# Kernel optimization log

Measured on AMD Instinct MI355X. Metric: run time of the kernel, lower is better.

The kernel has to match this reference:

```python
import jax, jax.numpy as jnp
import numpy as np
from jax import lax

# quantization bit widths (config)
IB, WB, RB, AB = 8, 4, 4, 8


def quantize(x, bw):
    """Signed fixed-point quantization to bw bits in [-1, 1) with STE."""
    scale = 2.0 ** (bw - 1)
    q = jnp.clip(jnp.round(x * scale), -scale, scale - 1) / scale
    return x + lax.stop_gradient(q - x)


def setup_inputs() -> dict:
    key = jax.random.key(0)
    k1, k2, k3, k4, k5 = jax.random.split(key, 5)
    B, T, I, H, O = 256, 1024, 64, 256, 16
    inputs = jax.random.normal(k1, (B, T, I), dtype=jnp.float32)
    # input kernel init: uniform(-1, 1)
    Wi = jax.random.uniform(k2, (H, I), dtype=jnp.float32, minval=-1.0, maxval=1.0)
    # recurrent kernel: orthogonal (geotorch parametrization); materialize via QR
    A = jax.random.normal(k3, (H, H), dtype=jnp.float32)
    Wr, _ = jnp.linalg.qr(A)
    Wr = Wr.astype(jnp.float32)
    Wo = jax.random.normal(k4, (O, H), dtype=jnp.float32) * 0.1
    b = jax.random.normal(k5, (H,), dtype=jnp.float32) * 0.01
    return {"inputs": inputs, "Wi": Wi, "Wr": Wr, "Wo": Wo, "b": b}


def reference(inputs, Wi, Wr, Wo, b):
    # quantize inputs (ib bits)
    x = quantize(inputs, IB)
    # quantized input projection, precomputed for all timesteps: [B,T,H]
    u = jnp.einsum("bti,hi->bth", x, quantize(Wi, WB))
    Wrq = quantize(Wr, RB)  # quantized orthogonal recurrent weight [H,H]
    B = inputs.shape[0]
    H = Wr.shape[0]
    h0 = jnp.zeros((B, H), dtype=inputs.dtype)

    def step(h, u_t):
        z = u_t + h @ Wrq.T                      # [B,H]
        m = jax.nn.relu(jnp.abs(z) + b)          # modrelu magnitude
        h_new = quantize(jnp.sign(z) * m, AB)    # quantized activation
        return h_new, None

    u_t = jnp.swapaxes(u, 0, 1)  # [T,B,H]
    h_last, _ = lax.scan(step, h0, u_t)
    # output head on last hidden state
    out = h_last @ quantize(Wo, WB).T  # [B,O]
    return out
```

## Files before the change

### kernel.cpp

```cpp
#include <hip/hip_runtime.h>


#define TSEQ 1024
#define IDIM 64
#define HDIM 256
#define ODIM 16

using i32x4 = __attribute__((ext_vector_type(4))) int;

__device__ __forceinline__ int sdot4i8(int a, int b, int c) {
#if __has_builtin(__builtin_amdgcn_sdot4)
    return __builtin_amdgcn_sdot4(a, b, c, false);
#else
    int r = c;
    r += ((a << 24) >> 24) * ((b << 24) >> 24);
    r += ((a << 16) >> 24) * ((b << 16) >> 24);
    r += ((a << 8)  >> 24) * ((b << 8)  >> 24);
    r += (a >> 24) * (b >> 24);
    return r;
#endif
}

__device__ __forceinline__ int qpack4(float4 f, float s, float lo, float hi) {
    int a = (int)fminf(fmaxf(rintf(f.x * s), lo), hi);
    int b = (int)fminf(fmaxf(rintf(f.y * s), lo), hi);
    int c = (int)fminf(fmaxf(rintf(f.z * s), lo), hi);
    int d = (int)fminf(fmaxf(rintf(f.w * s), lo), hi);
    return (a & 255) | ((b & 255) << 8) | ((c & 255) << 16) | ((d & 255) << 24);
}

__global__ __launch_bounds__(256, 1)
void qornn_kernel(const float* __restrict__ x, const float* __restrict__ Wi,
                  const float* __restrict__ Wr, const float* __restrict__ Wo,
                  const float* __restrict__ bias, float* __restrict__ out) {
    __shared__ alignas(16) int xlds[TSEQ * 16 + 16];
    __shared__ alignas(16) int wstage[8192];
    __shared__ alignas(16) int hbuf[2][64];

    const int tid = threadIdx.x;
    const int brow = blockIdx.x;
    const int w   = tid >> 6;
    const int l   = tid & 63;
    const int lm  = l & 15;
    const int lg  = l >> 4;
    const int olocal = ((l & 15) >> 2) * 16 + lg * 4 + (l & 3);
    const int oglob  = w * 64 + olocal;

    {
        const float4* wi4 = (const float4*)Wi;
        #pragma unroll
        for (int it = 0; it < 16; ++it) {
            int flat = it * 256 + tid;
            wstage[flat] = qpack4(wi4[flat], 8.0f, -8.0f, 7.0f);
        }
    }
    __syncthreads();
    int4 wi[4];
    {
        const int4* p = (const int4*)wstage;
        #pragma unroll
        for (int i = 0; i < 4; ++i) wi[i] = p[oglob * 4 + i];
    }
    __syncthreads();

    i32x4 wrA[4][4];
    {
        const float4* wr4 = (const float4*)Wr;
        #pragma unroll
        for (int it = 0; it < 32; ++it) {
            int flat = it * 256 + tid;
            wstage[flat] = qpack4(wr4[flat], 8.0f, -8.0f, 7.0f);
        }
        __syncthreads();
        if (w < 2) {
            const i32x4* p = (const i32x4*)wstage;
            #pragma unroll
            for (int tt = 0; tt < 4; ++tt)
                #pragma unroll
                for (int s = 0; s < 4; ++s)
                    wrA[tt][s] = p[(w * 64 + tt * 16 + lm) * 16 + s * 4 + lg];
        }
        __syncthreads();
        #pragma unroll
        for (int it = 0; it < 32; ++it) {
            int flat = it * 256 + tid;
            wstage[flat] = qpack4(wr4[8192 + flat], 8.0f, -8.0f, 7.0f);
        }
        __syncthreads();
        if (w >= 2) {
            const i32x4* p = (const i32x4*)wstage;
            #pragma unroll
            for (int tt = 0; tt < 4; ++tt)
                #pragma unroll
                for (int s = 0; s < 4; ++s)
                    wrA[tt][s] = p[((w - 2) * 64 + tt * 16 + lm) * 16 + s * 4 + lg];
        }
        __syncthreads();
    }

    {
        const float4* wo4 = (const float4*)Wo;
        #pragma unroll
        for (int it = 0; it < 4; ++it) {
            int flat = it * 256 + tid;
            wstage[flat] = qpack4(wo4[flat], 8.0f, -8.0f, 7.0f);
        }
    }

    {
        const float4* rowf4 = (const float4*)(x + (size_t)brow * (TSEQ * IDIM));
        #pragma unroll 8
        for (int it = 0; it < 64; ++it) {
            int flat = it * 256 + tid;
            xlds[flat] = qpack4(rowf4[flat], 128.0f, -128.0f, 127.0f);
        }
    }
    if (tid < 64) hbuf[0][tid] = 0;
    __syncthreads();

    const float bv = bias[oglob];
    const bool tb1 = (l & 8) != 0;
    const bool tb0 = (l & 4) != 0;
    const bool rb1 = (l & 2) != 0;
    const bool rb0 = (l & 1) != 0;

    int u = 0;
    #pragma unroll
    for (int s = 0; s < 4; ++s) {
        const int4 xx = ((const int4*)xlds)[s];
        u = sdot4i8(xx.x, wi[s].x, u);
        u = sdot4i8(xx.y, wi[s].y, u);
        u = sdot4i8(xx.z, wi[s].z, u);
        u = sdot4i8(xx.w, wi[s].w, u);
    }

    const i32x4 zero4 = {0, 0, 0, 0};

    #pragma unroll 2
    for (int t = 0; t < TSEQ; ++t) {
        i32x4 hB[4];
        {
            const i32x4* hP = (const i32x4*)hbuf[t & 1];
            #pragma unroll
            for (int s = 0; s < 4; ++s) hB[s] = hP[s * 4 + lg];
        }
        int4 xn[4];
        #pragma unroll
        for (int s = 0; s < 4; ++s) xn[s] = ((const int4*)xlds)[(t + 1) * 4 + s];

        i32x4 c0 = zero4, c1 = zero4, c2 = zero4, c3 = zero4;
        #pragma unroll
        for (int s = 0; s < 4; ++s) {
            c0 = __builtin_amdgcn_mfma_i32_16x16x64_i8(wrA[0][s], hB[s], c0, 0, 0, 0);
            c1 = __builtin_amdgcn_mfma_i32_16x16x64_i8(wrA[1][s], hB[s], c1, 0, 0, 0);
            c2 = __builtin_amdgcn_mfma_i32_16x16x64_i8(wrA[2][s], hB[s], c2, 0, 0, 0);
            c3 = __builtin_amdgcn_mfma_i32_16x16x64_i8(wrA[3][s], hB[s], c3, 0, 0, 0);
        }

        int un = 0;
        #pragma unroll
        for (int s = 0; s < 4; ++s) {
            un = sdot4i8(xn[s].x, wi[s].x, un);
            un = sdot4i8(xn[s].y, wi[s].y, un);
            un = sdot4i8(xn[s].z, wi[s].z, un);
            un = sdot4i8(xn[s].w, wi[s].w, un);
        }

        const i32x4 ca = tb1 ? c2 : c0;
        const i32x4 cb = tb1 ? c3 : c1;
        const i32x4 ct = tb0 ? cb : ca;
        const int zlo = rb1 ? ct[2] : ct[0];
        const int zhi = rb1 ? ct[3] : ct[1];
        const int z   = (rb0 ? zhi : zlo) + u;

        const float zf = (float)z;
        const float t1 = fmaf(fabsf(zf), 0.0009765625f, bv);
        const float t2 = fmaxf(t1, 0.0f);
        const float r  = rintf(t2 * 128.0f);
        const int vpos = (int)fminf(r, 127.0f);
        const int vneg = -(int)fminf(r, 128.0f);
        int hv = (z < 0) ? vneg : vpos;
        hv = (z == 0) ? 0 : hv;

        ((signed char*)hbuf[(t + 1) & 1])[oglob] = (signed char)hv;

        u = un;
        __syncthreads();
    }

    if (tid < ODIM) {
        const int4* wo = (const int4*)wstage;
        const int4* hl = (const int4*)hbuf[0];
        int a0 = 0, a1 = 0, a2 = 0, a3 = 0;
        #pragma unroll
        for (int i = 0; i < 16; ++i) {
            int4 w4 = wo[tid * 16 + i];
            int4 h4 = hl[i];
            a0 = sdot4i8(h4.x, w4.x, a0);
            a1 = sdot4i8(h4.y, w4.y, a1);
            a2 = sdot4i8(h4.z, w4.z, a2);
            a3 = sdot4i8(h4.w, w4.w, a3);
        }
        out[brow * ODIM + tid] = (float)((a0 + a1) + (a2 + a3)) * 0.0009765625f;
    }
}

extern "C" void kernel_launch(void* const* d_in, const int* in_sizes, int n_in,
                              void* d_out, int out_size, void* d_ws, size_t ws_size,
                              hipStream_t stream) {
    const float* x  = (const float*)d_in[0];
    const float* Wi = (const float*)d_in[1];
    const float* Wr = (const float*)d_in[2];
    const float* Wo = (const float*)d_in[3];
    const float* b  = (const float*)d_in[4];
    float* out = (float*)d_out;

    const int B = in_sizes[0] / (TSEQ * IDIM);
    qornn_kernel<<<B, HDIM, 0, stream>>>(x, Wi, Wr, Wo, b, out);
}
```

Measured before the change: 480.3 us.

## Replace MFMA recurrent matvec with per-thread sdot4 dot products

Each thread now owns one hidden unit. It keeps its full quantized Wr row (16 int4) in registers and computes the recurrent dot product with 64 sdot4 instructions across 8 independent accumulators, instead of using int8 MFMA tiles and then lane-selecting results. This removes the MFMA latency chain and the output-shuffling selects on the serial per-timestep critical path. In exchange each thread issues more VALU instructions and reads the whole 256-byte hidden vector from LDS every step. The input projection is also split into two partial sums, and the padding of the x buffer is enlarged.

```diff
diff --git a/kernel.cpp b/kernel.cpp
--- a/kernel.cpp
+++ b/kernel.cpp
@@ -5,8 +5,6 @@
 #define IDIM 64
 #define HDIM 256
 #define ODIM 16
-
-using i32x4 = __attribute__((ext_vector_type(4))) int;
 
 __device__ __forceinline__ int sdot4i8(int a, int b, int c) {
 #if __has_builtin(__builtin_amdgcn_sdot4)
@@ -33,18 +31,12 @@
 void qornn_kernel(const float* __restrict__ x, const float* __restrict__ Wi,
                   const float* __restrict__ Wr, const float* __restrict__ Wo,
                   const float* __restrict__ bias, float* __restrict__ out) {
-    __shared__ alignas(16) int xlds[TSEQ * 16 + 16];
+    __shared__ alignas(16) int xlds[TSEQ * 16 + 64];
     __shared__ alignas(16) int wstage[8192];
     __shared__ alignas(16) int hbuf[2][64];
 
     const int tid = threadIdx.x;
     const int brow = blockIdx.x;
-    const int w   = tid >> 6;
-    const int l   = tid & 63;
-    const int lm  = l & 15;
-    const int lg  = l >> 4;
-    const int olocal = ((l & 15) >> 2) * 16 + lg * 4 + (l & 3);
-    const int oglob  = w * 64 + olocal;
 
     {
         const float4* wi4 = (const float4*)Wi;
@@ -55,15 +47,15 @@
         }
     }
     __syncthreads();
-    int4 wi[4];
+    int4 wiq[4];
     {
         const int4* p = (const int4*)wstage;
         #pragma unroll
-        for (int i = 0; i < 4; ++i) wi[i] = p[oglob * 4 + i];
+        for (int r = 0; r < 4; ++r) wiq[r] = p[tid * 4 + r];
     }
     __syncthreads();
 
-    i32x4 wrA[4][4];
+    int4 wr[16];
     {
         const float4* wr4 = (const float4*)Wr;
         #pragma unroll
@@ -72,13 +64,10 @@
             wstage[flat] = qpack4(wr4[flat], 8.0f, -8.0f, 7.0f);
         }
         __syncthreads();
-        if (w < 2) {
-            const i32x4* p = (const i32x4*)wstage;
-            #pragma unroll
-            for (int tt = 0; tt < 4; ++tt)
-                #pragma unroll
-                for (int s = 0; s < 4; ++s)
-                    wrA[tt][s] = p[(w * 64 + tt * 16 + lm) * 16 + s * 4 + lg];
+        if (tid < 128) {
+            const int4* p = (const int4*)wstage;
+            #pragma unroll
+            for (int j = 0; j < 16; ++j) wr[j] = p[tid * 16 + j];
         }
         __syncthreads();
         #pragma unroll
@@ -87,13 +76,10 @@
             wstage[flat] = qpack4(wr4[8192 + flat], 8.0f, -8.0f, 7.0f);
         }
         __syncthreads();
-        if (w >= 2) {
-            const i32x4* p = (const i32x4*)wstage;
-            #pragma unroll
-            for (int tt = 0; tt < 4; ++tt)
-                #pragma unroll
-                for (int s = 0; s < 4; ++s)
-                    wrA[tt][s] = p[((w - 2) * 64 + tt * 16 + lm) * 16 + s * 4 + lg];
+        if (tid >= 128) {
+            const int4* p = (const int4*)wstage;
+            #pragma unroll
+            for (int j = 0; j < 16; ++j) wr[j] = p[(tid - 128) * 16 + j];
         }
         __syncthreads();
     }
@@ -118,60 +104,82 @@
     if (tid < 64) hbuf[0][tid] = 0;
     __syncthreads();
 
-    const float bv = bias[oglob];
-    const bool tb1 = (l & 8) != 0;
-    const bool tb0 = (l & 4) != 0;
-    const bool rb1 = (l & 2) != 0;
-    const bool rb0 = (l & 1) != 0;
-
-    int u = 0;
-    #pragma unroll
-    for (int s = 0; s < 4; ++s) {
-        const int4 xx = ((const int4*)xlds)[s];
-        u = sdot4i8(xx.x, wi[s].x, u);
-        u = sdot4i8(xx.y, wi[s].y, u);
-        u = sdot4i8(xx.z, wi[s].z, u);
-        u = sdot4i8(xx.w, wi[s].w, u);
-    }
-
-    const i32x4 zero4 = {0, 0, 0, 0};
+    const float bv = bias[tid];
+
+    int u;
+    {
+        const int4* xp = (const int4*)xlds;
+        int s0 = 0, s1 = 0;
+        #pragma unroll
+        for (int r = 0; r < 2; ++r) {
+            const int4 xx = xp[r];
+            s0 = sdot4i8(xx.x, wiq[r].x, s0);
+            s0 = sdot4i8(xx.y, wiq[r].y, s0);
+            s0 = sdot4i8(xx.z, wiq[r].z, s0);
+            s0 = sdot4i8(xx.w, wiq[r].w, s0);
+        }
+        #pragma unroll
+        for (int r = 2; r < 4; ++r) {
+            const int4 xx = xp[r];
+            s1 = sdot4i8(xx.x, wiq[r].x, s1);
+            s1 = sdot4i8(xx.y, wiq[r].y, s1);
+            s1 = sdot4i8(xx.z, wiq[r].z, s1);
+            s1 = sdot4i8(xx.w, wiq[r].w, s1);
+        }
+        u = s0 + s1;
+    }
 
     #pragma unroll 2
     for (int t = 0; t < TSEQ; ++t) {
-        i32x4 hB[4];
+        int4 hh[16];
         {
-            const i32x4* hP = (const i32x4*)hbuf[t & 1];
-            #pragma unroll
-            for (int s = 0; s < 4; ++s) hB[s] = hP[s * 4 + lg];
+            const int4* hP = (const int4*)hbuf[t & 1];
+            #pragma unroll
+            for (int j = 0; j < 16; ++j) hh[j] = hP[j];
         }
         int4 xn[4];
         #pragma unroll
-        for (int s = 0; s < 4; ++s) xn[s] = ((const int4*)xlds)[(t + 1) * 4 + s];
-
-        i32x4 c0 = zero4, c1 = zero4, c2 = zero4, c3 = zero4;
-        #pragma unroll
-        for (int s = 0; s < 4; ++s) {
-            c0 = __builtin_amdgcn_mfma_i32_16x16x64_i8(wrA[0][s], hB[s], c0, 0, 0, 0);
-            c1 = __builtin_amdgcn_mfma_i32_16x16x64_i8(wrA[1][s], hB[s], c1, 0, 0, 0);
-            c2 = __builtin_amdgcn_mfma_i32_16x16x64_i8(wrA[2][s], hB[s], c2, 0, 0, 0);
-            c3 = __builtin_amdgcn_mfma_i32_16x16x64_i8(wrA[3][s], hB[s], c3, 0, 0, 0);
-        }
-
-        int un = 0;
-        #pragma unroll
-        for (int s = 0; s < 4; ++s) {
-            un = sdot4i8(xn[s].x, wi[s].x, un);
-            un = sdot4i8(xn[s].y, wi[s].y, un);
-            un = sdot4i8(xn[s].z, wi[s].z, un);
-            un = sdot4i8(xn[s].w, wi[s].w, un);
-        }
-
-        const i32x4 ca = tb1 ? c2 : c0;
-        const i32x4 cb = tb1 ? c3 : c1;
-        const i32x4 ct = tb0 ? cb : ca;
-        const int zlo = rb1 ? ct[2] : ct[0];
-        const int zhi = rb1 ? ct[3] : ct[1];
-        const int z   = (rb0 ? zhi : zlo) + u;
+        for (int r = 0; r < 4; ++r) xn[r] = ((const int4*)xlds)[(t + 1) * 4 + r];
+
+        int a0 = u, a1 = 0, a2 = 0, a3 = 0, a4 = 0, a5 = 0, a6 = 0, a7 = 0;
+        #pragma unroll
+        for (int c = 0; c < 8; ++c) {
+            int s = (c == 0) ? a0 : ((c == 1) ? a1 : (c == 2) ? a2 : (c == 3) ? a3
+                  : (c == 4) ? a4 : (c == 5) ? a5 : (c == 6) ? a6 : a7);
+            s = sdot4i8(hh[c].x, wr[c].x, s);
+            s = sdot4i8(hh[c].y, wr[c].y, s);
+            s = sdot4i8(hh[c].z, wr[c].z, s);
+            s = sdot4i8(hh[c].w, wr[c].w, s);
+            s = sdot4i8(hh[c + 8].x, wr[c + 8].x, s);
+            s = sdot4i8(hh[c + 8].y, wr[c + 8].y, s);
+            s = sdot4i8(hh[c + 8].z, wr[c + 8].z, s);
+            s = sdot4i8(hh[c + 8].w, wr[c + 8].w, s);
+            if (c == 0) a0 = s; else if (c == 1) a1 = s; else if (c == 2) a2 = s;
+            else if (c == 3) a3 = s; else if (c == 4) a4 = s; else if (c == 5) a5 = s;
+            else if (c == 6) a6 = s; else a7 = s;
+        }
+
+        int un;
+        {
+            int s0 = 0, s1 = 0;
+            #pragma unroll
+            for (int r = 0; r < 2; ++r) {
+                s0 = sdot4i8(xn[r].x, wiq[r].x, s0);
+                s0 = sdot4i8(xn[r].y, wiq[r].y, s0);
+                s0 = sdot4i8(xn[r].z, wiq[r].z, s0);
+                s0 = sdot4i8(xn[r].w, wiq[r].w, s0);
+            }
+            #pragma unroll
+            for (int r = 2; r < 4; ++r) {
+                s1 = sdot4i8(xn[r].x, wiq[r].x, s1);
+                s1 = sdot4i8(xn[r].y, wiq[r].y, s1);
+                s1 = sdot4i8(xn[r].z, wiq[r].z, s1);
+                s1 = sdot4i8(xn[r].w, wiq[r].w, s1);
+            }
+            un = s0 + s1;
+        }
+
+        const int z = ((a0 + a1) + (a2 + a3)) + ((a4 + a5) + (a6 + a7));
 
         const float zf = (float)z;
         const float t1 = fmaf(fabsf(zf), 0.0009765625f, bv);
@@ -182,7 +190,7 @@
         int hv = (z < 0) ? vneg : vpos;
         hv = (z == 0) ? 0 : hv;
 
-        ((signed char*)hbuf[(t + 1) & 1])[oglob] = (signed char)hv;
+        ((signed char*)hbuf[(t + 1) & 1])[tid] = (signed char)hv;
 
         u = un;
         __syncthreads();
```

Measured after the change: 518.4 us. 7.9% more time.
